# Performance work log

Hardware: AMD Instinct MI355X
Metric: run time of the kernel (lower is better)

Reference implementation:

```python
import jax, jax.numpy as jnp
import numpy as np

B, N, C_IN, T = 16, 1024, 16, 36
K, C_OUT = 3, 64


def setup_inputs() -> dict:
    key = jax.random.key(0)
    k1, k2, k3, k4 = jax.random.split(key, 4)
    x = jax.random.normal(k1, (B, N, C_IN, T), dtype=jnp.float32)
    spatial_attention = jax.random.uniform(k2, (B, N, N), dtype=jnp.float32)
    cheb = jax.random.normal(k3, (K, N, N), dtype=jnp.float32) * 0.1
    theta = jax.random.normal(k4, (K, C_IN, C_OUT), dtype=jnp.float32) * 0.1
    return {"x": x, "spatial_attention": spatial_attention, "cheb": cheb, "theta": theta}


def reference(x, spatial_attention, cheb, theta):
    # x: [B,N,C_in,T], spatial_attention: [B,N,N], cheb: [K,N,N], theta: [K,C_in,C_out]
    # Original: per (t,k): ((T_k * SAt).T @ x[..., t]) @ theta_k, summed over k, ReLU.
    # Compute attention-weighted adjacency ONCE (time-invariant), batch over all t.
    t_at = cheb[:, None, :, :] * spatial_attention[None]          # [K,B,N,N]
    # rhs[k,b,n,c,t] = sum_m t_at[k,b,m,n] * x[b,m,c,t]  (permute(0,2,1).matmul)
    rhs = jnp.einsum('kbmn,bmct->kbnct', t_at, x)                 # [K,B,N,C_in,T]
    out = jnp.einsum('kbnct,kco->bnot', rhs, theta)               # [B,N,C_out,T]
    return jax.nn.relu(out)
```

## Files before the change

kernel.cpp:

```cpp
#include <hip/hip_runtime.h>
#include <hip/hip_bf16.h>

#define NB 16
#define NN 1024
#define CIN 16
#define TT 36
#define KK 3
#define COUT 64
#define CT 576
#define KB 48

typedef __attribute__((ext_vector_type(8))) short bf16x8;
typedef __attribute__((ext_vector_type(4))) float f32x4;

__device__ __forceinline__ unsigned short f2bf(float f) {
    union { float f; unsigned int u; } v; v.f = f;
    unsigned int r = v.u + 0x7FFF + ((v.u >> 16) & 1);
    return (unsigned short)(r >> 16);
}

__global__ __launch_bounds__(256) void prep_a(const float* __restrict__ cheb,
                                              const float* __restrict__ sat,
                                              ushort* __restrict__ At,
                                              int n_base, int rows) {
    __shared__ ushort tile[64][68];
    const int ntiles = rows >> 6;
    const int k = blockIdx.y;
    const int n0 = n_base + (blockIdx.x % ntiles) * 64;
    const int m0 = (blockIdx.x / ntiles) * 64;
    const int tid = threadIdx.x;

    size_t goff[4];
    float4 cv[4], sv[4];
#pragma unroll
    for (int i = 0; i < 4; ++i) {
        int f = i * 256 + tid;
        goff[i] = (size_t)(m0 + (f >> 4)) * NN + n0 + ((f & 15) << 2);
        cv[i] = *(const float4*)(cheb + (size_t)k * NN * NN + goff[i]);
        sv[i] = *(const float4*)(sat + goff[i]);
    }
    for (int b = 0; b < 16; ++b) {
#pragma unroll
        for (int i = 0; i < 4; ++i) {
            int f = i * 256 + tid;
            ushort4 u;
            u.x = f2bf(cv[i].x * sv[i].x); u.y = f2bf(cv[i].y * sv[i].y);
            u.z = f2bf(cv[i].z * sv[i].z); u.w = f2bf(cv[i].w * sv[i].w);
            *(ushort4*)&tile[f >> 4][(f & 15) << 2] = u;
        }
        if (b < 15) {
            const float* sa = sat + (size_t)(b + 1) * NN * NN;
#pragma unroll
            for (int i = 0; i < 4; ++i) sv[i] = *(const float4*)(sa + goff[i]);
        }
        __syncthreads();
        ushort* outp = At + (size_t)(k * 16 + b) * rows * NN;
#pragma unroll
        for (int i = 0; i < 4; ++i) {
            int f = i * 256 + tid;
            int n = f >> 4, m4 = (f & 15) << 2;
            ushort4 u;
            u.x = tile[m4 + 0][n]; u.y = tile[m4 + 1][n];
            u.z = tile[m4 + 2][n]; u.w = tile[m4 + 3][n];
            *(ushort4*)(outp + (size_t)(n0 - n_base + n) * NN + m0 + m4) = u;
        }
        __syncthreads();
    }
}

__global__ __launch_bounds__(256) void prep_x(const float* __restrict__ x,
                                              ushort* __restrict__ Xt) {
    __shared__ ushort tile[64][68];
    const int b = blockIdx.y;
    const int m0 = (blockIdx.x & 15) * 64;
    const int c0 = (blockIdx.x >> 4) * 64;
    const int tid = threadIdx.x;
    const float* xb = x + (size_t)b * NN * CT;
#pragma unroll
    for (int i = 0; i < 4; ++i) {
        int f = i * 256 + tid;
        int mr = f >> 4, c4 = (f & 15) << 2;
        float4 v = *(const float4*)(xb + (size_t)(m0 + mr) * CT + c0 + c4);
        ushort4 u;
        u.x = f2bf(v.x); u.y = f2bf(v.y); u.z = f2bf(v.z); u.w = f2bf(v.w);
        *(ushort4*)&tile[mr][c4] = u;
    }
    __syncthreads();
    ushort* outp = Xt + (size_t)b * CT * NN;
#pragma unroll
    for (int i = 0; i < 4; ++i) {
        int f = i * 256 + tid;
        int n = f >> 4, m4 = (f & 15) << 2;
        int ctlin = c0 + n;
        int c = ctlin / 36, t = ctlin - 36 * c;
        int ctp = t * 16 + c;
        ushort4 u;
        u.x = tile[m4 + 0][n]; u.y = tile[m4 + 1][n];
        u.z = tile[m4 + 2][n]; u.w = tile[m4 + 3][n];
        *(ushort4*)(outp + (size_t)ctp * NN + m0 + m4) = u;
    }
}

__global__ __launch_bounds__(256) void gemm1(const ushort* __restrict__ At,
                                             const ushort* __restrict__ Xt,
                                             ushort* __restrict__ rhs2,
                                             int nsplit, int n_base, int rows) {
    __shared__ ushort smem[128 * 200];
    ushort* lA = smem;
    ushort* lB = smem + 128 * 64;
    const int tid = threadIdx.x;
    const int y = blockIdx.y;
    const int b = y / 3, k = y - 3 * b;
    const int l = k * 16 + b;
    const int ntiles = rows >> 7;
    const int nt = blockIdx.x % ntiles;
    const int ctt = blockIdx.x / ntiles;
    const int nloc0 = nt * 128;
    const int ct0 = ctt * 192;
    const ushort* Ab = At + ((size_t)l * (nsplit ? rows : NN) + nloc0) * NN;
    const ushort* Bb = Xt + (size_t)b * CT * NN + (size_t)ct0 * NN;
    const int w = tid >> 6, lane = tid & 63;
    const int wr = w >> 1, wc = w & 1;
    const int lrow = lane & 15, quad = lane >> 4;
    f32x4 acc[4][6] = {};

    for (int kt = 0; kt < 16; ++kt) {
        const int mk = kt * 64;
#pragma unroll
        for (int i = 0; i < 4; ++i) {
            int f = i * 256 + tid;
            int row = f >> 3, kk = (f & 7) << 3;
            __builtin_amdgcn_global_load_lds(
                (const __attribute__((address_space(1))) void*)(Ab + (size_t)row * NN + mk + kk),
                (__attribute__((address_space(3))) void*)(&lA[f * 8]), 16, 0, 0);
        }
#pragma unroll
        for (int i = 0; i < 6; ++i) {
            int f = i * 256 + tid;
            int row = f >> 3, kk = (f & 7) << 3;
            __builtin_amdgcn_global_load_lds(
                (const __attribute__((address_space(1))) void*)(Bb + (size_t)row * NN + mk + kk),
                (__attribute__((address_space(3))) void*)(&lB[f * 8]), 16, 0, 0);
        }
        __syncthreads();
#pragma unroll
        for (int kk0 = 0; kk0 < 64; kk0 += 32) {
            bf16x8 af[4], bfr[6];
#pragma unroll
            for (int mi = 0; mi < 4; ++mi)
                af[mi] = *(const bf16x8*)&lA[(wr * 64 + mi * 16 + lrow) * 64 + kk0 + quad * 8];
#pragma unroll
            for (int ni = 0; ni < 6; ++ni)
                bfr[ni] = *(const bf16x8*)&lB[(wc * 96 + ni * 16 + lrow) * 64 + kk0 + quad * 8];
#pragma unroll
            for (int mi = 0; mi < 4; ++mi)
#pragma unroll
                for (int ni = 0; ni < 6; ++ni)
                    acc[mi][ni] = __builtin_amdgcn_mfma_f32_16x16x32_bf16(
                        af[mi], bfr[ni], acc[mi][ni], 0, 0, 0);
        }
        __syncthreads();
    }

#pragma unroll
    for (int mi = 0; mi < 4; ++mi)
#pragma unroll
        for (int ni = 0; ni < 6; ++ni)
#pragma unroll
            for (int r = 0; r < 4; ++r)
                smem[(wr * 64 + mi * 16 + quad * 4 + r) * 200 + wc * 96 + ni * 16 + lrow] =
                    f2bf(acc[mi][ni][r]);
    __syncthreads();

    for (int f = tid; f < 1536; f += 256) {
        int n = f / 12, tl = f - 12 * (f / 12);
        int t = ctt * 12 + tl;
        uint4 v0 = *(const uint4*)&smem[n * 200 + tl * 16];
        uint4 v1 = *(const uint4*)&smem[n * 200 + tl * 16 + 8];
        size_t g = (((size_t)b * NN + n_base + nloc0 + n) * 36 + t) * 48 + k * 16;
        *(uint4*)(rhs2 + g) = v0;
        *(uint4*)(rhs2 + g + 8) = v1;
    }
}

__global__ __launch_bounds__(256) void apply_mfma2(const ushort* __restrict__ rhs2,
                                                   const float* __restrict__ theta,
                                                   float* __restrict__ out) {
    __shared__ ushort thT[64 * 72];
    __shared__ float ostage[4][64 * 36];
    const int tid = threadIdx.x;
    for (int f = tid; f < 64 * 64; f += 256) {
        int o = f >> 6, kc = f & 63;
        thT[o * 72 + kc] = f2bf((kc < 48) ? theta[kc * 64 + o] : 0.f);
    }
    __syncthreads();
    const int w = tid >> 6, lane = tid & 63;
    const int lrow = lane & 15, quad = lane >> 4;

    bf16x8 a[4][2];
#pragma unroll
    for (int mi = 0; mi < 4; ++mi)
#pragma unroll
        for (int kc = 0; kc < 2; ++kc)
            a[mi][kc] = *(const bf16x8*)&thT[(mi * 16 + lrow) * 72 + kc * 32 + quad * 8];

    float* ost = &ostage[w][0];
    for (int j = 0; j < 4; ++j) {
        const int bn = blockIdx.x * 16 + w * 4 + j;
        const ushort* rrow = rhs2 + (size_t)bn * (36 * 48);
        f32x4 acc[4][3] = {};
#pragma unroll
        for (int ni = 0; ni < 3; ++ni)
#pragma unroll
            for (int kc = 0; kc < 2; ++kc) {
                bf16x8 bf = *(const bf16x8*)(rrow + (ni * 16 + lrow) * 48 + kc * 32 + quad * 8);
#pragma unroll
                for (int mi = 0; mi < 4; ++mi)
                    acc[mi][ni] = __builtin_amdgcn_mfma_f32_16x16x32_bf16(
                        a[mi][kc], bf, acc[mi][ni], 0, 0, 0);
            }
#pragma unroll
        for (int mi = 0; mi < 4; ++mi)
#pragma unroll
            for (int ni = 0; ni < 3; ++ni)
#pragma unroll
                for (int r = 0; r < 4; ++r) {
                    int t = ni * 16 + lrow;
                    if (t < 36)
                        ost[(mi * 16 + quad * 4 + r) * 36 + t] = fmaxf(acc[mi][ni][r], 0.f);
                }
        asm volatile("s_waitcnt lgkmcnt(0)" ::: "memory");
        float* ob = out + (size_t)bn * (COUT * TT);
#pragma unroll
        for (int q = 0; q < 9; ++q) {
            int f = q * 64 + lane;
            *(float4*)&ob[f * 4] = *(const float4*)&ost[f * 4];
        }
    }
}

__global__ __launch_bounds__(256) void naive_fused(const float* __restrict__ x,
                                                   const float* __restrict__ sat,
                                                   const float* __restrict__ cheb,
                                                   const float* __restrict__ theta,
                                                   float* __restrict__ out) {
    __shared__ float wgt[3][1024];
    __shared__ float rs[3][576];
    const int tid = threadIdx.x;
    const int n = blockIdx.x, b = blockIdx.y;
    for (int f = tid; f < 3 * 1024; f += 256) {
        int k = f >> 10, m = f & 1023;
        wgt[k][m] = cheb[(size_t)k * NN * NN + (size_t)m * NN + n] *
                    sat[(size_t)b * NN * NN + (size_t)m * NN + n];
    }
    __syncthreads();
    float a0[3] = {}, a1[3] = {}, a2[3] = {};
    const float* xb = x + (size_t)b * NN * CT;
    for (int m = 0; m < 1024; ++m) {
        const float* xr = xb + (size_t)m * CT;
        float x0 = xr[tid];
        float x1 = xr[256 + tid];
        float x2 = (tid < 64) ? xr[512 + tid] : 0.f;
#pragma unroll
        for (int k = 0; k < 3; ++k) {
            float wm = wgt[k][m];
            a0[k] += wm * x0; a1[k] += wm * x1; a2[k] += wm * x2;
        }
    }
#pragma unroll
    for (int k = 0; k < 3; ++k) {
        rs[k][tid] = a0[k];
        rs[k][256 + tid] = a1[k];
        if (tid < 64) rs[k][512 + tid] = a2[k];
    }
    __syncthreads();
    const int o = tid >> 2, tg = tid & 3;
    float oa[9] = {};
    for (int kc = 0; kc < 48; ++kc) {
        int k = kc >> 4, c = kc & 15;
        float th = theta[kc * 64 + o];
        const float* rp = &rs[k][c * TT + tg * 9];
#pragma unroll
        for (int j = 0; j < 9; ++j) oa[j] += th * rp[j];
    }
    float* ob = out + ((size_t)b * NN + n) * (COUT * TT);
#pragma unroll
    for (int j = 0; j < 9; ++j)
        ob[o * TT + tg * 9 + j] = fmaxf(oa[j], 0.f);
}

extern "C" void kernel_launch(void* const* d_in, const int* in_sizes, int n_in,
                              void* d_out, int out_size, void* d_ws, size_t ws_size,
                              hipStream_t stream) {
    const float* x     = (const float*)d_in[0];
    const float* sat   = (const float*)d_in[1];
    const float* cheb  = (const float*)d_in[2];
    const float* theta = (const float*)d_in[3];
    float* out = (float*)d_out;

    const size_t RHS2 = (size_t)NB * NN * 36 * 48;
    const size_t XT   = (size_t)NB * CT * NN;
    const size_t ATF  = (size_t)KB * NN * NN;
    const size_t ATNS = (size_t)KB * 512 * NN;
    const size_t needA     = (RHS2 + XT + ATF) * 2;
    const size_t needSplit = (RHS2 + XT + ATNS) * 2;

    ushort* rhs2 = (ushort*)d_ws;
    ushort* Xt   = rhs2 + RHS2;
    ushort* At   = Xt + XT;

    if (ws_size >= needA) {
        prep_x<<<dim3(144, NB), 256, 0, stream>>>(x, Xt);
        prep_a<<<dim3(256, KK), 256, 0, stream>>>(cheb, sat, At, 0, 1024);
        gemm1<<<dim3(24, KB), 256, 0, stream>>>(At, Xt, rhs2, 0, 0, 1024);
        apply_mfma2<<<dim3(NB * NN / 16), 256, 0, stream>>>(rhs2, theta, out);
    } else if (ws_size >= needSplit) {
        prep_x<<<dim3(144, NB), 256, 0, stream>>>(x, Xt);
        for (int half = 0; half < 2; ++half) {
            int nb = half * 512;
            prep_a<<<dim3(128, KK), 256, 0, stream>>>(cheb, sat, At, nb, 512);
            gemm1<<<dim3(12, KB), 256, 0, stream>>>(At, Xt, rhs2, 1, nb, 512);
        }
        apply_mfma2<<<dim3(NB * NN / 16), 256, 0, stream>>>(rhs2, theta, out);
    } else {
        naive_fused<<<dim3(NN, NB), 256, 0, stream>>>(x, sat, cheb, theta, out);
    }
}
```

Before: 405.5 us.

## Double-buffer gemm1 LDS tiles with swizzle and 512-thread blocks

Reworks the main GEMM kernel to use 512 threads (8 waves, each owning a 64x48 output tile) and a two-stage LDS ping-pong buffer, so global-to-LDS loads for tile kt+2 are issued while tile kt is being computed. The LDS layout is XOR-swizzled to cut bank conflicts on fragment reads, and MFMA sections raise wave priority. This targets the load-then-compute serialization and LDS conflicts of the old single-buffer loop. In exchange it uses roughly 80KB of LDS per block, which may lower occupancy, and it depends on hand-written waitcnt/barrier sequencing being correct.

```diff
diff --git a/kernel.cpp b/kernel.cpp
--- a/kernel.cpp
+++ b/kernel.cpp
@@ -101,13 +101,11 @@
     }
 }
 
-__global__ __launch_bounds__(256) void gemm1(const ushort* __restrict__ At,
+__global__ __launch_bounds__(512) void gemm1(const ushort* __restrict__ At,
                                              const ushort* __restrict__ Xt,
                                              ushort* __restrict__ rhs2,
                                              int nsplit, int n_base, int rows) {
-    __shared__ ushort smem[128 * 200];
-    ushort* lA = smem;
-    ushort* lB = smem + 128 * 64;
+    __shared__ ushort lds[2 * 320 * 64];
     const int tid = threadIdx.x;
     const int y = blockIdx.y;
     const int b = y / 3, k = y - 3 * b;
@@ -119,64 +117,88 @@
     const int ct0 = ctt * 192;
     const ushort* Ab = At + ((size_t)l * (nsplit ? rows : NN) + nloc0) * NN;
     const ushort* Bb = Xt + (size_t)b * CT * NN + (size_t)ct0 * NN;
+
+    const int srow = tid >> 3;
+    const int schunk = tid & 7;
+    const int swz = schunk ^ (srow & 7);
+    const ushort* a_src0 = Ab + (size_t)srow * NN + swz * 8;
+    const ushort* b_src0 = Bb + (size_t)srow * NN + swz * 8;
+
+    auto STAGE = [&](int kt, int p) {
+        const int mk = kt * 64;
+        ushort* base = lds + p * (320 * 64);
+        const ushort* as = a_src0 + mk;
+        const ushort* bs = b_src0 + mk;
+#pragma unroll
+        for (int i = 0; i < 2; ++i)
+            __builtin_amdgcn_global_load_lds(
+                (const __attribute__((address_space(1))) void*)(as + (size_t)i * 64 * NN),
+                (__attribute__((address_space(3))) void*)(base + (tid + i * 512) * 8), 16, 0, 0);
+#pragma unroll
+        for (int i = 0; i < 3; ++i)
+            __builtin_amdgcn_global_load_lds(
+                (const __attribute__((address_space(1))) void*)(bs + (size_t)i * 64 * NN),
+                (__attribute__((address_space(3))) void*)(base + 128 * 64 + (tid + i * 512) * 8), 16, 0, 0);
+    };
+
     const int w = tid >> 6, lane = tid & 63;
-    const int wr = w >> 1, wc = w & 1;
+    const int wr = w >> 2, wc = w & 3;
     const int lrow = lane & 15, quad = lane >> 4;
-    f32x4 acc[4][6] = {};
+    const int koff0 = ((quad ^ (lrow & 7)) << 3);
+    f32x4 acc[4][3] = {};
+
+    STAGE(0, 0);
+    STAGE(1, 1);
+    asm volatile("s_waitcnt vmcnt(5)\n\ts_barrier" ::: "memory");
 
     for (int kt = 0; kt < 16; ++kt) {
-        const int mk = kt * 64;
-#pragma unroll
-        for (int i = 0; i < 4; ++i) {
-            int f = i * 256 + tid;
-            int row = f >> 3, kk = (f & 7) << 3;
-            __builtin_amdgcn_global_load_lds(
-                (const __attribute__((address_space(1))) void*)(Ab + (size_t)row * NN + mk + kk),
-                (__attribute__((address_space(3))) void*)(&lA[f * 8]), 16, 0, 0);
-        }
-#pragma unroll
-        for (int i = 0; i < 6; ++i) {
-            int f = i * 256 + tid;
-            int row = f >> 3, kk = (f & 7) << 3;
-            __builtin_amdgcn_global_load_lds(
-                (const __attribute__((address_space(1))) void*)(Bb + (size_t)row * NN + mk + kk),
-                (__attribute__((address_space(3))) void*)(&lB[f * 8]), 16, 0, 0);
-        }
-        __syncthreads();
-#pragma unroll
-        for (int kk0 = 0; kk0 < 64; kk0 += 32) {
-            bf16x8 af[4], bfr[6];
+        const int p = kt & 1;
+        const ushort* bufA = lds + p * (320 * 64);
+        const ushort* bufB = bufA + 128 * 64;
+#pragma unroll
+        for (int kp = 0; kp < 2; ++kp) {
+            const int koff = koff0 ^ (kp << 5);
+            bf16x8 af[4], bfr[3];
 #pragma unroll
             for (int mi = 0; mi < 4; ++mi)
-                af[mi] = *(const bf16x8*)&lA[(wr * 64 + mi * 16 + lrow) * 64 + kk0 + quad * 8];
-#pragma unroll
-            for (int ni = 0; ni < 6; ++ni)
-                bfr[ni] = *(const bf16x8*)&lB[(wc * 96 + ni * 16 + lrow) * 64 + kk0 + quad * 8];
+                af[mi] = *(const bf16x8*)&bufA[(wr * 64 + mi * 16 + lrow) * 64 + koff];
+#pragma unroll
+            for (int ni = 0; ni < 3; ++ni)
+                bfr[ni] = *(const bf16x8*)&bufB[(wc * 48 + ni * 16 + lrow) * 64 + koff];
+            __builtin_amdgcn_s_setprio(1);
 #pragma unroll
             for (int mi = 0; mi < 4; ++mi)
 #pragma unroll
-                for (int ni = 0; ni < 6; ++ni)
+                for (int ni = 0; ni < 3; ++ni)
                     acc[mi][ni] = __builtin_amdgcn_mfma_f32_16x16x32_bf16(
                         af[mi], bfr[ni], acc[mi][ni], 0, 0, 0);
-        }
-        __syncthreads();
-    }
-
+            __builtin_amdgcn_s_setprio(0);
+        }
+        asm volatile("s_barrier" ::: "memory");
+        if (kt + 2 < 16) {
+            STAGE(kt + 2, p);
+            asm volatile("s_waitcnt vmcnt(5)\n\ts_barrier" ::: "memory");
+        } else if (kt + 1 < 16) {
+            asm volatile("s_waitcnt vmcnt(0)\n\ts_barrier" ::: "memory");
+        }
+    }
+
+    ushort* cs = lds;
 #pragma unroll
     for (int mi = 0; mi < 4; ++mi)
 #pragma unroll
-        for (int ni = 0; ni < 6; ++ni)
+        for (int ni = 0; ni < 3; ++ni)
 #pragma unroll
             for (int r = 0; r < 4; ++r)
-                smem[(wr * 64 + mi * 16 + quad * 4 + r) * 200 + wc * 96 + ni * 16 + lrow] =
+                cs[(wr * 64 + mi * 16 + quad * 4 + r) * 200 + wc * 48 + ni * 16 + lrow] =
                     f2bf(acc[mi][ni][r]);
     __syncthreads();
 
-    for (int f = tid; f < 1536; f += 256) {
+    for (int f = tid; f < 1536; f += 512) {
         int n = f / 12, tl = f - 12 * (f / 12);
         int t = ctt * 12 + tl;
-        uint4 v0 = *(const uint4*)&smem[n * 200 + tl * 16];
-        uint4 v1 = *(const uint4*)&smem[n * 200 + tl * 16 + 8];
+        uint4 v0 = *(const uint4*)&cs[n * 200 + tl * 16];
+        uint4 v1 = *(const uint4*)&cs[n * 200 + tl * 16 + 8];
         size_t g = (((size_t)b * NN + n_base + nloc0 + n) * 36 + t) * 48 + k * 16;
         *(uint4*)(rhs2 + g) = v0;
         *(uint4*)(rhs2 + g + 8) = v1;
@@ -312,14 +334,14 @@
     if (ws_size >= needA) {
         prep_x<<<dim3(144, NB), 256, 0, stream>>>(x, Xt);
         prep_a<<<dim3(256, KK), 256, 0, stream>>>(cheb, sat, At, 0, 1024);
-        gemm1<<<dim3(24, KB), 256, 0, stream>>>(At, Xt, rhs2, 0, 0, 1024);
+        gemm1<<<dim3(24, KB), 512, 0, stream>>>(At, Xt, rhs2, 0, 0, 1024);
         apply_mfma2<<<dim3(NB * NN / 16), 256, 0, stream>>>(rhs2, theta, out);
     } else if (ws_size >= needSplit) {
         prep_x<<<dim3(144, NB), 256, 0, stream>>>(x, Xt);
         for (int half = 0; half < 2; ++half) {
             int nb = half * 512;
             prep_a<<<dim3(128, KK), 256, 0, stream>>>(cheb, sat, At, nb, 512);
-            gemm1<<<dim3(12, KB), 256, 0, stream>>>(At, Xt, rhs2, 1, nb, 512);
+            gemm1<<<dim3(12, KB), 512, 0, stream>>>(At, Xt, rhs2, 1, nb, 512);
         }
         apply_mfma2<<<dim3(NB * NN / 16), 256, 0, stream>>>(rhs2, theta, out);
     } else {
```

Result: faster. 384.9 us (-5.1%).
